# Kernel tuning notes

Measured on AMD Instinct MI355X. Metric: run time of the kernel, lower is better.

Reference implementation:

```python
import jax, jax.numpy as jnp
import numpy as np

EPS = 1e-5
NEG = -1e9

def rmsnorm(x, g, eps=EPS):
    x32 = x.astype(jnp.float32)
    n = x32 * jax.lax.rsqrt(jnp.mean(x32 * x32, axis=-1, keepdims=True) + eps)
    return g * n.astype(x.dtype)

def setup_inputs() -> dict:
    key = jax.random.key(0)
    ks = jax.random.split(key, 10)
    B, S, D, H = 2, 2048, 768, 12
    F = 4 * D
    s = 0.02
    return {
        "x": jax.random.normal(ks[0], (B, S, D), jnp.float32),
        "mask": jax.random.randint(ks[1], (B, S, S), 0, 2, jnp.int32),
        "wq": jax.random.normal(ks[2], (D, D), jnp.float32) * s,
        "wk": jax.random.normal(ks[3], (D, D), jnp.float32) * s,
        "wv": jax.random.normal(ks[4], (D, D), jnp.float32) * s,
        "wo": jax.random.normal(ks[5], (D, D), jnp.float32) * s,
        "w1": jax.random.normal(ks[6], (F, D), jnp.float32) * s,
        "w2": jax.random.normal(ks[7], (D, F), jnp.float32) * s,
        "w3": jax.random.normal(ks[8], (F, D), jnp.float32) * s,
        "g_attn": jnp.ones((D,), jnp.float32),
        "g_ffn": jnp.ones((D,), jnp.float32),
    }

def reference(x, mask, wq, wk, wv, wo, w1, w2, w3, g_attn, g_ffn):
    B, S, D = x.shape
    H = 12
    Dk = D // H
    # --- attention sub-block (pre-norm) ---
    xn = rmsnorm(x, g_attn)
    # torch Linear: y = x @ W^T; split heads -> [B,H,S,Dk]
    q = (xn @ wq.T).reshape(B, S, H, Dk).transpose(0, 2, 1, 3)
    k = (xn @ wk.T).reshape(B, S, H, Dk).transpose(0, 2, 1, 3)
    v = (xn @ wv.T).reshape(B, S, H, Dk).transpose(0, 2, 1, 3)
    scores = jnp.einsum("bhqd,bhkd->bhqk", q, k) / jnp.sqrt(jnp.float32(Dk))
    scores = jnp.where(mask[:, None, :, :] == 0, jnp.float32(NEG), scores)
    probs = jax.nn.softmax(scores, axis=-1)  # dropout p=0.0 -> identity
    attn = jnp.einsum("bhqk,bhkd->bhqd", probs, v)
    attn = attn.transpose(0, 2, 1, 3).reshape(B, S, D)
    h = x + attn @ wo.T
    # --- SwiGLU FFN sub-block (pre-norm) ---
    hn = rmsnorm(h, g_ffn)
    ffn = (jax.nn.silu(hn @ w1.T) * (hn @ w3.T)) @ w2.T
    return h + ffn
```

## Files before the change

### kernel.cpp

```cpp
#include <hip/hip_runtime.h>
#include <hip/hip_bf16.h>

#define S_LEN 2048
#define D_MODEL 768
#define NH 12
#define DK 64
#define F_DIM 3072
#define BATCH 2
#define M_ROWS (BATCH * S_LEN)

typedef __bf16 bf16x8 __attribute__((ext_vector_type(8)));
typedef float floatx4 __attribute__((ext_vector_type(4)));
typedef unsigned short u16;
typedef unsigned long long u64;

__device__ inline float bf2f(u16 u) {
    union { unsigned int i; float f; } x; x.i = ((unsigned int)u) << 16; return x.f;
}
__device__ inline u16 f2bf(float f) {
    union { float f; unsigned int i; } x; x.f = f;
    unsigned int r = x.i + 0x7fffu + ((x.i >> 16) & 1u);
    return (u16)(r >> 16);
}
__device__ __forceinline__ bf16x8 as_bf16x8(uint4 v) {
    union { uint4 u; bf16x8 b; } c; c.u = v; return c.b;
}

__device__ __forceinline__ void ldsload16(const u16* g, u16* l) {
    __builtin_amdgcn_global_load_lds(
        (const __attribute__((address_space(1))) unsigned int*)g,
        (__attribute__((address_space(3))) unsigned int*)l, 16, 0, 0);
}

__global__ __launch_bounds__(256)
void cvt_all(const float4* __restrict__ wq, const float4* __restrict__ wk,
             const float4* __restrict__ wv, const float4* __restrict__ wo,
             const float4* __restrict__ w1, const float4* __restrict__ w2,
             const float4* __restrict__ w3,
             ushort4* wqb, ushort4* wkb, ushort4* wvb, ushort4* wob,
             ushort4* w13f, ushort4* w2b) {
    const int WS4 = (D_MODEL * D_MODEL) / 4;
    const int WB4 = (F_DIM * D_MODEL) / 4;
    const int RW4 = D_MODEL / 4;
    int i = blockIdx.x * 256 + threadIdx.x;
    const float4* src; ushort4* dst; int off, doff;
    if (i < 4 * WS4) {
        int s = i / WS4; off = i - s * WS4; doff = off;
        src = (s == 0) ? wq : (s == 1) ? wk : (s == 2) ? wv : wo;
        dst = (s == 0) ? wqb : (s == 1) ? wkb : (s == 2) ? wvb : wob;
    } else {
        int j = i - 4 * WS4; int s = j / WB4; off = j - s * WB4;
        if (s == 1) { src = w2; dst = w2b; doff = off; }
        else {
            src = (s == 0) ? w1 : w3;
            dst = w13f;
            int which = (s == 0) ? 0 : 1;
            int row = off / RW4, c4 = off - row * RW4;
            int k = c4 * 4;
            int n_tile = row >> 4, nl = row & 15;
            int k_tile = k >> 5, quad = (k >> 3) & 3, jj = k & 7;
            int lane = quad * 16 + nl;
            int f = (n_tile * 24 + k_tile) * 2 + which;
            doff = (f * 512 + lane * 8 + jj) >> 2;
        }
    }
    float4 v = src[off];
    ushort4 o;
    o.x = f2bf(v.x); o.y = f2bf(v.y); o.z = f2bf(v.z); o.w = f2bf(v.w);
    dst[doff] = o;
}

__global__ __launch_bounds__(256)
void mask_bits(const int* __restrict__ m, u64* __restrict__ bits) {
    size_t base = (size_t)blockIdx.x * 2048 + threadIdx.x;
    #pragma unroll
    for (int it = 0; it < 8; ++it) {
        size_t gid = base + (size_t)it * 256;
        u64 b = __ballot(m[gid] != 0);
        if ((threadIdx.x & 63) == 0) bits[gid >> 6] = b;
    }
}

__global__ __launch_bounds__(256)
void rmsnorm_k(const float* __restrict__ x, const float* __restrict__ g, u16* __restrict__ out) {
    int row = blockIdx.x;
    const float* xr = x + (size_t)row * D_MODEL;
    u16* orow = out + (size_t)row * D_MODEL;
    int t = threadIdx.x;
    float v0 = xr[t];
    float v1 = xr[t + 256];
    float v2 = xr[t + 512];
    float ss = v0 * v0 + v1 * v1 + v2 * v2;
    #pragma unroll
    for (int off = 1; off < 64; off <<= 1) ss += __shfl_xor(ss, off);
    __shared__ float red[4];
    if ((t & 63) == 0) red[t >> 6] = ss;
    __syncthreads();
    float tot = red[0] + red[1] + red[2] + red[3];
    float scale = rsqrtf(tot * (1.0f / (float)D_MODEL) + 1e-5f);
    orow[t]       = f2bf(g[t]       * v0 * scale);
    orow[t + 256] = f2bf(g[t + 256] * v1 * scale);
    orow[t + 512] = f2bf(g[t + 512] * v2 * scale);
}

__global__ __launch_bounds__(256, 3)
void gemm_f1(const u16* __restrict__ A, const u16* __restrict__ W13f,
             u16* __restrict__ Cout) {
    const int K = D_MODEL, N = F_DIM;
    __shared__ u16 As[2][64][64];

    int t = threadIdx.x;
    int w = t >> 6, lane = t & 63;
    int lrow = lane & 15, quad = lane >> 4;

    int lid = blockIdx.y * 24 + blockIdx.x;
    int xcd = lid & 7, s = lid >> 3;
    int nb = xcd * 3 + (s % 3);
    int mb = s / 3;
    int mBase = mb * 64;
    int ntile0 = nb * 8 + w * 2;

    int srow8 = lane >> 3;
    int sc64 = ((lane & 7) ^ srow8) * 8;
    const u16* Ag = A + (size_t)(mBase + w * 16 + srow8) * K + sc64;
    const uint4* Bf = (const uint4*)W13f;

    auto stageA = [&](int k0, int b) {
        ldsload16(Ag + k0,                 &As[b][w * 16][0]);
        ldsload16(Ag + (size_t)8 * K + k0, &As[b][w * 16 + 8][0]);
    };

    floatx4 zero = {0.f, 0.f, 0.f, 0.f};
    floatx4 acc[4][2], acc2[4][2];
    #pragma unroll
    for (int r = 0; r < 4; ++r)
        #pragma unroll
        for (int c = 0; c < 2; ++c) { acc[r][c] = zero; acc2[r][c] = zero; }

    stageA(0, 0);
    int cur = 0;
    for (int kt2 = 0; kt2 < 12; ++kt2) {
        uint4 b1v[2][2], b3v[2][2];
        #pragma unroll
        for (int hh = 0; hh < 2; ++hh) {
            int kt = kt2 * 2 + hh;
            #pragma unroll
            for (int c = 0; c < 2; ++c) {
                int f = ((ntile0 + c) * 24 + kt) * 2;
                b1v[hh][c] = Bf[(size_t)f * 64 + lane];
                b3v[hh][c] = Bf[(size_t)(f + 1) * 64 + lane];
            }
        }
        __syncthreads();
        if (kt2 + 1 < 12) stageA((kt2 + 1) * 64, cur ^ 1);

        #pragma unroll
        for (int hh = 0; hh < 2; ++hh) {
            int rc = ((hh * 4 + quad) ^ (lrow & 7)) * 8;
            bf16x8 af[4];
            #pragma unroll
            for (int r = 0; r < 4; ++r) af[r] = *(const bf16x8*)&As[cur][r * 16 + lrow][rc];
            #pragma unroll
            for (int c = 0; c < 2; ++c) {
                bf16x8 b1f = as_bf16x8(b1v[hh][c]);
                bf16x8 b3f = as_bf16x8(b3v[hh][c]);
                #pragma unroll
                for (int r = 0; r < 4; ++r) {
                    acc[r][c]  = __builtin_amdgcn_mfma_f32_16x16x32_bf16(af[r], b1f, acc[r][c], 0, 0, 0);
                    acc2[r][c] = __builtin_amdgcn_mfma_f32_16x16x32_bf16(af[r], b3f, acc2[r][c], 0, 0, 0);
                }
            }
        }
        cur ^= 1;
    }

    #pragma unroll
    for (int r = 0; r < 4; ++r) {
        #pragma unroll
        for (int c = 0; c < 2; ++c) {
            #pragma unroll
            for (int j = 0; j < 4; ++j) {
                int grow = mBase + r * 16 + quad * 4 + j;
                int gcol = nb * 128 + w * 32 + c * 16 + lrow;
                float a = acc[r][c][j];
                Cout[(size_t)grow * N + gcol] = f2bf((a / (1.0f + __expf(-a))) * acc2[r][c][j]);
            }
        }
    }
}

__global__ __launch_bounds__(256, 3)
void gemm64(const u16* __restrict__ A, const u16* __restrict__ B1,
            const float* __restrict__ R, float* __restrict__ Cout, int N, int K) {
    __shared__ u16 As[2][64][64];
    __shared__ u16 Bs[2][64][64];

    int t = threadIdx.x;
    int w = t >> 6, lane = t & 63;

    int L = blockIdx.y * gridDim.x + blockIdx.x;
    int xcd = L & 7;
    int i = L >> 3;
    int nT = gridDim.x;
    int mPer = gridDim.y >> 3;
    int nIdx = i % nT;
    int mIdx = xcd * mPer + i / nT;
    int mBase = mIdx * 64, nBase = nIdx * 64;

    int lrow = lane & 15, quad = lane >> 4;
    int wm = (w >> 1) * 32, wn = (w & 1) * 32;

    int srow8 = lane >> 3;
    int sc64 = ((lane & 7) ^ srow8) * 8;
    const u16* Ag = A  + (size_t)(mBase + w * 16 + srow8) * K + sc64;
    const u16* Bg = B1 + (size_t)(nBase + w * 16 + srow8) * K + sc64;

    auto stage = [&](int k0, int b) {
        ldsload16(Ag + k0,                 &As[b][w * 16][0]);
        ldsload16(Ag + (size_t)8 * K + k0, &As[b][w * 16 + 8][0]);
        ldsload16(Bg + k0,                 &Bs[b][w * 16][0]);
        ldsload16(Bg + (size_t)8 * K + k0, &Bs[b][w * 16 + 8][0]);
    };

    floatx4 zero = {0.f, 0.f, 0.f, 0.f};
    floatx4 acc[2][2];
    #pragma unroll
    for (int r = 0; r < 2; ++r)
        #pragma unroll
        for (int c = 0; c < 2; ++c) acc[r][c] = zero;

    stage(0, 0);
    int cur = 0;
    for (int k0 = 0; k0 < K; k0 += 64) {
        __syncthreads();
        if (k0 + 64 < K) stage(k0 + 64, cur ^ 1);

        #pragma unroll
        for (int half = 0; half < 2; ++half) {
            int rc = ((half * 4 + quad) ^ (lrow & 7)) * 8;
            bf16x8 af[2], bf[2];
            #pragma unroll
            for (int r = 0; r < 2; ++r) af[r] = *(const bf16x8*)&As[cur][wm + r * 16 + lrow][rc];
            #pragma unroll
            for (int c = 0; c < 2; ++c) bf[c] = *(const bf16x8*)&Bs[cur][wn + c * 16 + lrow][rc];
            #pragma unroll
            for (int r = 0; r < 2; ++r)
                #pragma unroll
                for (int c = 0; c < 2; ++c)
                    acc[r][c] = __builtin_amdgcn_mfma_f32_16x16x32_bf16(af[r], bf[c], acc[r][c], 0, 0, 0);
        }
        cur ^= 1;
    }

    #pragma unroll
    for (int r = 0; r < 2; ++r) {
        #pragma unroll
        for (int c = 0; c < 2; ++c) {
            #pragma unroll
            for (int j = 0; j < 4; ++j) {
                int grow = mBase + wm + r * 16 + quad * 4 + j;
                int gcol = nBase + wn + c * 16 + lrow;
                size_t idx = (size_t)grow * N + gcol;
                Cout[idx] = acc[r][c][j] + R[idx];
            }
        }
    }
}

__global__ __launch_bounds__(256, 4)
void gemm_qkv(const u16* __restrict__ A, const u16* __restrict__ wq,
              const u16* __restrict__ wk, const u16* __restrict__ wv,
              u16* __restrict__ qb, u16* __restrict__ kb, u16* __restrict__ vt) {
    const int K = D_MODEL;
    __shared__ u16 As[2][64][32];
    __shared__ u16 Bs[2][128][32];

    int t = threadIdx.x;
    int w = t >> 6, lane = t & 63;

    int L = blockIdx.y * 18 + blockIdx.x;
    int g = (L & 7) * 144 + (L >> 3);
    int xI = g >> 6;
    int yI = g & 63;
    int which = xI / 6;
    int mBase = yI * 64, nBase = (xI % 6) * 128;
    const u16* B1 = (which == 0) ? wq : (which == 1) ? wk : wv;
    int lrow = lane & 15, quad = lane >> 4;
    int wm = (w >> 1) * 32, wn = (w & 1) * 64;

    int srow = lane >> 2;
    int scolS = ((lane & 3) ^ ((lane >> 3) & 3)) * 8;
    int rq = (quad ^ ((lrow >> 1) & 3)) * 8;
    const u16* Ag = A  + (size_t)(mBase + w * 16 + srow) * K + scolS;
    const u16* Bg = B1 + (size_t)(nBase + w * 32 + srow) * K + scolS;

    auto stage = [&](int k0, int b) {
        ldsload16(Ag + k0, &As[b][w * 16][0]);
        ldsload16(Bg + k0, &Bs[b][w * 32][0]);
        ldsload16(Bg + (size_t)16 * K + k0, &Bs[b][w * 32 + 16][0]);
    };

    floatx4 zero = {0.f, 0.f, 0.f, 0.f};
    floatx4 acc[2][4];
    #pragma unroll
    for (int r = 0; r < 2; ++r)
        #pragma unroll
        for (int c = 0; c < 4; ++c) acc[r][c] = zero;

    stage(0, 0);
    int cur = 0;
    for (int k0 = 0; k0 < K; k0 += 32) {
        __syncthreads();
        if (k0 + 32 < K) stage(k0 + 32, cur ^ 1);
        bf16x8 af[2];
        #pragma unroll
        for (int r = 0; r < 2; ++r) af[r] = *(const bf16x8*)&As[cur][wm + r * 16 + lrow][rq];
        #pragma unroll
        for (int c = 0; c < 4; ++c) {
            bf16x8 bfr = *(const bf16x8*)&Bs[cur][wn + c * 16 + lrow][rq];
            #pragma unroll
            for (int r = 0; r < 2; ++r)
                acc[r][c] = __builtin_amdgcn_mfma_f32_16x16x32_bf16(af[r], bfr, acc[r][c], 0, 0, 0);
        }
        cur ^= 1;
    }

    u16* dst = (which == 0) ? qb : kb;
    const float qscale = 0.18033688011112042f;
    #pragma unroll
    for (int r = 0; r < 2; ++r) {
        #pragma unroll
        for (int c = 0; c < 4; ++c) {
            #pragma unroll
            for (int j = 0; j < 4; ++j) {
                int grow = mBase + wm + r * 16 + quad * 4 + j;
                int gcol = nBase + wn + c * 16 + lrow;
                float val = acc[r][c][j];
                if (which == 2) {
                    int bb = grow >> 11, s = grow & 2047;
                    int hh = gcol >> 6, d = gcol & 63;
                    vt[((((size_t)bb * NH + hh) * DK + d) << 11) + s] = f2bf(val);
                } else {
                    if (which == 0) val *= qscale;
                    dst[(size_t)grow * D_MODEL + gcol] = f2bf(val);
                }
            }
        }
    }
}

__global__ __launch_bounds__(256)
void attn_mfma(const u16* __restrict__ q, const u16* __restrict__ k,
               const u16* __restrict__ vt, const u64* __restrict__ mbits,
               u16* __restrict__ out) {
    __shared__ u16 Ks0[2][64][32], Ks1[2][64][32];
    __shared__ u16 Vs0[2][64][32], Vs1[2][64][32];
    __shared__ u16 PT[4][16][64];

    int t = threadIdx.x;
    int lane = t & 63;
    int w = t >> 6;
    int lrow = lane & 15;
    int quad = lane >> 4;

    int L = blockIdx.y * gridDim.x + blockIdx.x;
    int g = (L & 7) * 96 + (L >> 3);
    int st0 = (g & 31) * 64;
    int bh = g >> 5;
    int h = bh % NH;
    int b = bh / NH;

    const u16* kbase = k + (size_t)b * S_LEN * D_MODEL + h * DK;
    const u16* vbase = vt + (size_t)bh * DK * S_LEN;
    const u64* bw = mbits + ((size_t)b * S_LEN + st0 + w * 16 + lrow) * (S_LEN / 64);

    int srow = lane >> 2;
    int scolS = ((lane & 3) ^ ((lane >> 3) & 3)) * 8;
    int rq = (quad ^ ((lrow >> 1) & 3)) * 8;
    int ptw = lrow & 7;
    int rp0 = (quad ^ ptw) * 8;
    int rp1 = ((4 + quad) ^ ptw) * 8;
    int pqo = (quad & 1) * 4;
    int pch = quad >> 1;

    const u16* kg = kbase + (size_t)(w * 16 + srow) * D_MODEL + scolS;
    const u16* vg = vbase + (size_t)(w * 16 + srow) * S_LEN + scolS;

    auto stageKV = [&](int kt, int bsel) {
        ldsload16(kg + (size_t)kt * D_MODEL,      &Ks0[bsel][w * 16][0]);
        ldsload16(kg + (size_t)kt * D_MODEL + 32, &Ks1[bsel][w * 16][0]);
        ldsload16(vg + kt,      &Vs0[bsel][w * 16][0]);
        ldsload16(vg + kt + 32, &Vs1[bsel][w * 16][0]);
    };

    stageKV(0, 0);

    bf16x8 bq0, bq1;
    {
        const u16* qrow = q + ((size_t)b * S_LEN + st0 + w * 16 + lrow) * D_MODEL + h * DK + quad * 8;
        bq0 = *(const bf16x8*)qrow;
        bq1 = *(const bf16x8*)(qrow + 32);
    }

    bf16x8 ones;
    {
        union { u16 u; __bf16 b; } o; o.u = 0x3F80;
        #pragma unroll
        for (int j = 0; j < 8; ++j) ones[j] = o.b;
    }

    floatx4 zero = {0.f, 0.f, 0.f, 0.f};
    floatx4 Ot[4] = {zero, zero, zero, zero};
    floatx4 Osum = zero;

    u64 mw = bw[0];
    __syncthreads();

    int cur = 0;
    for (int kt = 0; kt < S_LEN; kt += 64) {
        if (kt + 64 < S_LEN) stageKV(kt + 64, cur ^ 1);
        u64 mw_next = (kt + 64 < S_LEN) ? bw[(kt >> 6) + 1] : 0ull;
        unsigned mlo = (unsigned)mw, mhi = (unsigned)(mw >> 32);

        floatx4 st[4];
        #pragma unroll
        for (int nt = 0; nt < 4; ++nt) {
            bf16x8 ak0 = *(const bf16x8*)&Ks0[cur][nt * 16 + lrow][rq];
            bf16x8 ak1 = *(const bf16x8*)&Ks1[cur][nt * 16 + lrow][rq];
            st[nt] = __builtin_amdgcn_mfma_f32_16x16x32_bf16(ak0, bq0, zero, 0, 0, 0);
            st[nt] = __builtin_amdgcn_mfma_f32_16x16x32_bf16(ak1, bq1, st[nt], 0, 0, 0);
        }

        #pragma unroll
        for (int nt = 0; nt < 4; ++nt) {
            unsigned half = (nt & 2) ? mhi : mlo;
            unsigned tmp = half >> ((nt & 1) * 16 + quad * 4);
            unsigned eu[4];
            #pragma unroll
            for (int j = 0; j < 4; ++j) {
                float e = __builtin_amdgcn_exp2f(st[nt][j]);
                unsigned msk = (unsigned)((int)(tmp << (31 - j)) >> 31);
                eu[j] = __float_as_uint(e) & msk;
            }
            uint2 p;
            p.x = (eu[0] >> 16) | (eu[1] & 0xffff0000u);
            p.y = (eu[2] >> 16) | (eu[3] & 0xffff0000u);
            int pc = ((nt * 2 + pch) ^ ptw) * 8 + pqo;
            *(uint2*)&PT[w][lrow][pc] = p;
        }

        bf16x8 ap0 = *(const bf16x8*)&PT[w][lrow][rp0];
        bf16x8 ap1 = *(const bf16x8*)&PT[w][lrow][rp1];
        Osum = __builtin_amdgcn_mfma_f32_16x16x32_bf16(ap0, ones, Osum, 0, 0, 0);
        Osum = __builtin_amdgcn_mfma_f32_16x16x32_bf16(ap1, ones, Osum, 0, 0, 0);
        #pragma unroll
        for (int dt = 0; dt < 4; ++dt) {
            bf16x8 bv0 = *(const bf16x8*)&Vs0[cur][dt * 16 + lrow][rq];
            bf16x8 bv1 = *(const bf16x8*)&Vs1[cur][dt * 16 + lrow][rq];
            Ot[dt] = __builtin_amdgcn_mfma_f32_16x16x32_bf16(ap0, bv0, Ot[dt], 0, 0, 0);
            Ot[dt] = __builtin_amdgcn_mfma_f32_16x16x32_bf16(ap1, bv1, Ot[dt], 0, 0, 0);
        }

        __syncthreads();
        cur ^= 1;
        mw = mw_next;
    }

    float invj[4];
    #pragma unroll
    for (int j = 0; j < 4; ++j) invj[j] = 1.0f / Osum[j];

    u16* obase = out + ((size_t)b * S_LEN + st0 + w * 16) * D_MODEL + h * DK;
    #pragma unroll
    for (int dt = 0; dt < 4; ++dt)
        #pragma unroll
        for (int j = 0; j < 4; ++j)
            obase[(size_t)(quad * 4 + j) * D_MODEL + dt * 16 + lrow] = f2bf(Ot[dt][j] * invj[j]);
}

extern "C" void kernel_launch(void* const* d_in, const int* in_sizes, int n_in,
                              void* d_out, int out_size, void* d_ws, size_t ws_size,
                              hipStream_t stream) {
    const float* x      = (const float*)d_in[0];
    const int*   mask   = (const int*)d_in[1];
    const float* wq     = (const float*)d_in[2];
    const float* wk     = (const float*)d_in[3];
    const float* wv     = (const float*)d_in[4];
    const float* wo     = (const float*)d_in[5];
    const float* w1     = (const float*)d_in[6];
    const float* w2     = (const float*)d_in[7];
    const float* w3     = (const float*)d_in[8];
    const float* g_attn = (const float*)d_in[9];
    const float* g_ffn  = (const float*)d_in[10];
    float* out = (float*)d_out;

    const size_t WSMALL = (size_t)D_MODEL * D_MODEL;
    const size_t WBIG   = (size_t)F_DIM * D_MODEL;
    const size_t MD     = (size_t)M_ROWS * D_MODEL;

    char* ws = (char*)d_ws;
    u16* wqb  = (u16*)ws;            ws += WSMALL * 2;
    u16* wkb  = (u16*)ws;            ws += WSMALL * 2;
    u16* wvb  = (u16*)ws;            ws += WSMALL * 2;
    u16* wob  = (u16*)ws;            ws += WSMALL * 2;
    u16* w13f = (u16*)ws;            ws += WBIG * 2 * 2;
    u16* w2b  = (u16*)ws;            ws += WBIG * 2;
    u16* xn  = (u16*)ws;             ws += MD * 2;
    u16* qb  = (u16*)ws;             ws += MD * 2;
    u16* kb  = (u16*)ws;             ws += MD * 2;
    u16* vb  = (u16*)ws;             ws += MD * 2;
    u16* ao  = (u16*)ws;             ws += MD * 2;
    float* hb = (float*)ws;          ws += MD * 4;
    u64* mb  = (u64*)ws;             ws += (size_t)BATCH * S_LEN * (S_LEN / 64) * 8;
    u16* hn = xn;
    u16* ub = qb;
    (void)ws_size; (void)n_in; (void)in_sizes; (void)out_size;

    dim3 blk(256);

    cvt_all<<<9216, blk, 0, stream>>>((const float4*)wq, (const float4*)wk, (const float4*)wv,
                                      (const float4*)wo, (const float4*)w1, (const float4*)w2,
                                      (const float4*)w3,
                                      (ushort4*)wqb, (ushort4*)wkb, (ushort4*)wvb, (ushort4*)wob,
                                      (ushort4*)w13f, (ushort4*)w2b);
    mask_bits<<<(BATCH * S_LEN * S_LEN) / 2048, blk, 0, stream>>>(mask, mb);

    rmsnorm_k<<<M_ROWS, blk, 0, stream>>>(x, g_attn, xn);
    gemm_qkv<<<dim3(18, M_ROWS / 64), blk, 0, stream>>>(xn, wqb, wkb, wvb, qb, kb, vb);
    attn_mfma<<<dim3(S_LEN / 64, BATCH * NH), blk, 0, stream>>>(qb, kb, vb, mb, ao);
    gemm64<<<dim3(D_MODEL / 64, M_ROWS / 64), blk, 0, stream>>>(ao, wob, x, hb, D_MODEL, D_MODEL);
    rmsnorm_k<<<M_ROWS, blk, 0, stream>>>((const float*)hb, g_ffn, hn);
    gemm_f1<<<dim3(24, M_ROWS / 64), blk, 0, stream>>>(hn, w13f, ub);
    gemm64<<<dim3(D_MODEL / 64, M_ROWS / 64), blk, 0, stream>>>(ub, w2b, hb, out, D_MODEL, F_DIM);
}
```

Baseline: 327.6 us.

## Merge prep kernels and switch QKV GEMM to fragment-packed weights

The weight conversion, mask bit-packing and first RMSNorm now run as one combined launch, so two kernel launches and their gaps disappear. Wq/Wk/Wv are converted into one MFMA-fragment-ordered buffer. The QKV GEMM then loads B fragments straight from global memory into registers, with no LDS staging, and stages only A through LDS with a 64-wide K tile and XOR swizzle. This trades LDS traffic and barriers for direct global loads of B, and changes the warp tiling to 64x32 per warp.

```diff
diff --git a/kernel.cpp b/kernel.cpp
--- a/kernel.cpp
+++ b/kernel.cpp
@@ -32,22 +32,30 @@
         (__attribute__((address_space(3))) unsigned int*)l, 16, 0, 0);
 }
 
-__global__ __launch_bounds__(256)
-void cvt_all(const float4* __restrict__ wq, const float4* __restrict__ wk,
-             const float4* __restrict__ wv, const float4* __restrict__ wo,
-             const float4* __restrict__ w1, const float4* __restrict__ w2,
-             const float4* __restrict__ w3,
-             ushort4* wqb, ushort4* wkb, ushort4* wvb, ushort4* wob,
-             ushort4* w13f, ushort4* w2b) {
+__device__ __forceinline__ void cvt_body(
+        int i,
+        const float4* wq, const float4* wk, const float4* wv, const float4* wo,
+        const float4* w1, const float4* w2, const float4* w3,
+        ushort4* wqkvf, ushort4* wob, ushort4* w13f, ushort4* w2b) {
     const int WS4 = (D_MODEL * D_MODEL) / 4;
     const int WB4 = (F_DIM * D_MODEL) / 4;
     const int RW4 = D_MODEL / 4;
-    int i = blockIdx.x * 256 + threadIdx.x;
     const float4* src; ushort4* dst; int off, doff;
     if (i < 4 * WS4) {
-        int s = i / WS4; off = i - s * WS4; doff = off;
+        int s = i / WS4; off = i - s * WS4;
         src = (s == 0) ? wq : (s == 1) ? wk : (s == 2) ? wv : wo;
-        dst = (s == 0) ? wqb : (s == 1) ? wkb : (s == 2) ? wvb : wob;
+        if (s == 3) { dst = wob; doff = off; }
+        else {
+            dst = wqkvf;
+            int row = off / RW4, c4 = off - row * RW4;
+            int k = c4 * 4;
+            int rg = s * D_MODEL + row;
+            int n_tile = rg >> 4, nl = rg & 15;
+            int k_tile = k >> 5, qd = (k >> 3) & 3, jj = k & 7;
+            int ln = qd * 16 + nl;
+            int f = n_tile * 24 + k_tile;
+            doff = (f * 512 + ln * 8 + jj) >> 2;
+        }
     } else {
         int j = i - 4 * WS4; int s = j / WB4; off = j - s * WB4;
         if (s == 1) { src = w2; dst = w2b; doff = off; }
@@ -58,10 +66,10 @@
             int row = off / RW4, c4 = off - row * RW4;
             int k = c4 * 4;
             int n_tile = row >> 4, nl = row & 15;
-            int k_tile = k >> 5, quad = (k >> 3) & 3, jj = k & 7;
-            int lane = quad * 16 + nl;
+            int k_tile = k >> 5, qd = (k >> 3) & 3, jj = k & 7;
+            int ln = qd * 16 + nl;
             int f = (n_tile * 24 + k_tile) * 2 + which;
-            doff = (f * 512 + lane * 8 + jj) >> 2;
+            doff = (f * 512 + ln * 8 + jj) >> 2;
         }
     }
     float4 v = src[off];
@@ -70,9 +78,8 @@
     dst[doff] = o;
 }
 
-__global__ __launch_bounds__(256)
-void mask_bits(const int* __restrict__ m, u64* __restrict__ bits) {
-    size_t base = (size_t)blockIdx.x * 2048 + threadIdx.x;
+__device__ __forceinline__ void mask_body(int bx, const int* m, u64* bits) {
+    size_t base = (size_t)bx * 2048 + threadIdx.x;
     #pragma unroll
     for (int it = 0; it < 8; ++it) {
         size_t gid = base + (size_t)it * 256;
@@ -81,9 +88,8 @@
     }
 }
 
-__global__ __launch_bounds__(256)
-void rmsnorm_k(const float* __restrict__ x, const float* __restrict__ g, u16* __restrict__ out) {
-    int row = blockIdx.x;
+__device__ __forceinline__ void rms_body(int row, const float* x, const float* g,
+                                         u16* out, float* red) {
     const float* xr = x + (size_t)row * D_MODEL;
     u16* orow = out + (size_t)row * D_MODEL;
     int t = threadIdx.x;
@@ -93,7 +99,6 @@
     float ss = v0 * v0 + v1 * v1 + v2 * v2;
     #pragma unroll
     for (int off = 1; off < 64; off <<= 1) ss += __shfl_xor(ss, off);
-    __shared__ float red[4];
     if ((t & 63) == 0) red[t >> 6] = ss;
     __syncthreads();
     float tot = red[0] + red[1] + red[2] + red[3];
@@ -101,6 +106,30 @@
     orow[t]       = f2bf(g[t]       * v0 * scale);
     orow[t + 256] = f2bf(g[t + 256] * v1 * scale);
     orow[t + 512] = f2bf(g[t + 512] * v2 * scale);
+}
+
+__global__ __launch_bounds__(256)
+void prep(const float4* wq, const float4* wk, const float4* wv, const float4* wo,
+          const float4* w1, const float4* w2, const float4* w3,
+          ushort4* wqkvf, ushort4* wob, ushort4* w13f, ushort4* w2b,
+          const int* m, u64* bits,
+          const float* x, const float* g, u16* xn) {
+    __shared__ float red[4];
+    int bx = blockIdx.x;
+    if (bx < 9216) {
+        cvt_body(bx * 256 + threadIdx.x, wq, wk, wv, wo, w1, w2, w3,
+                 wqkvf, wob, w13f, w2b);
+    } else if (bx < 13312) {
+        mask_body(bx - 9216, m, bits);
+    } else {
+        rms_body(bx - 13312, x, g, xn, red);
+    }
+}
+
+__global__ __launch_bounds__(256)
+void rmsnorm_k(const float* __restrict__ x, const float* __restrict__ g, u16* __restrict__ out) {
+    __shared__ float red[4];
+    rms_body(blockIdx.x, x, g, out, red);
 }
 
 __global__ __launch_bounds__(256, 3)
@@ -268,81 +297,91 @@
 }
 
 __global__ __launch_bounds__(256, 4)
-void gemm_qkv(const u16* __restrict__ A, const u16* __restrict__ wq,
-              const u16* __restrict__ wk, const u16* __restrict__ wv,
+void gemm_qkv(const u16* __restrict__ A, const u16* __restrict__ Wf,
               u16* __restrict__ qb, u16* __restrict__ kb, u16* __restrict__ vt) {
     const int K = D_MODEL;
-    __shared__ u16 As[2][64][32];
-    __shared__ u16 Bs[2][128][32];
+    __shared__ u16 As[2][64][64];
 
     int t = threadIdx.x;
     int w = t >> 6, lane = t & 63;
+    int lrow = lane & 15, quad = lane >> 4;
 
     int L = blockIdx.y * 18 + blockIdx.x;
     int g = (L & 7) * 144 + (L >> 3);
-    int xI = g >> 6;
-    int yI = g & 63;
-    int which = xI / 6;
-    int mBase = yI * 64, nBase = (xI % 6) * 128;
-    const u16* B1 = (which == 0) ? wq : (which == 1) ? wk : wv;
-    int lrow = lane & 15, quad = lane >> 4;
-    int wm = (w >> 1) * 32, wn = (w & 1) * 64;
-
-    int srow = lane >> 2;
-    int scolS = ((lane & 3) ^ ((lane >> 3) & 3)) * 8;
-    int rq = (quad ^ ((lrow >> 1) & 3)) * 8;
-    const u16* Ag = A  + (size_t)(mBase + w * 16 + srow) * K + scolS;
-    const u16* Bg = B1 + (size_t)(nBase + w * 32 + srow) * K + scolS;
-
-    auto stage = [&](int k0, int b) {
-        ldsload16(Ag + k0, &As[b][w * 16][0]);
-        ldsload16(Bg + k0, &Bs[b][w * 32][0]);
-        ldsload16(Bg + (size_t)16 * K + k0, &Bs[b][w * 32 + 16][0]);
+    int nb = g >> 6;
+    int mBase = (g & 63) * 64;
+    int ntile0 = nb * 8 + w * 2;
+
+    int srow8 = lane >> 3;
+    int sc64 = ((lane & 7) ^ srow8) * 8;
+    const u16* Ag = A + (size_t)(mBase + w * 16 + srow8) * K + sc64;
+    const uint4* Bf = (const uint4*)Wf;
+
+    auto stageA = [&](int k0, int b) {
+        ldsload16(Ag + k0,                 &As[b][w * 16][0]);
+        ldsload16(Ag + (size_t)8 * K + k0, &As[b][w * 16 + 8][0]);
     };
 
     floatx4 zero = {0.f, 0.f, 0.f, 0.f};
-    floatx4 acc[2][4];
-    #pragma unroll
-    for (int r = 0; r < 2; ++r)
-        #pragma unroll
-        for (int c = 0; c < 4; ++c) acc[r][c] = zero;
-
-    stage(0, 0);
+    floatx4 acc[4][2];
+    #pragma unroll
+    for (int r = 0; r < 4; ++r)
+        #pragma unroll
+        for (int c = 0; c < 2; ++c) acc[r][c] = zero;
+
+    stageA(0, 0);
     int cur = 0;
-    for (int k0 = 0; k0 < K; k0 += 32) {
+    for (int kt2 = 0; kt2 < 12; ++kt2) {
+        uint4 bv[2][2];
+        #pragma unroll
+        for (int hh = 0; hh < 2; ++hh) {
+            int kt = kt2 * 2 + hh;
+            #pragma unroll
+            for (int c = 0; c < 2; ++c) {
+                int f = (ntile0 + c) * 24 + kt;
+                bv[hh][c] = Bf[(size_t)f * 64 + lane];
+            }
+        }
         __syncthreads();
-        if (k0 + 32 < K) stage(k0 + 32, cur ^ 1);
-        bf16x8 af[2];
-        #pragma unroll
-        for (int r = 0; r < 2; ++r) af[r] = *(const bf16x8*)&As[cur][wm + r * 16 + lrow][rq];
-        #pragma unroll
-        for (int c = 0; c < 4; ++c) {
-            bf16x8 bfr = *(const bf16x8*)&Bs[cur][wn + c * 16 + lrow][rq];
-            #pragma unroll
-            for (int r = 0; r < 2; ++r)
-                acc[r][c] = __builtin_amdgcn_mfma_f32_16x16x32_bf16(af[r], bfr, acc[r][c], 0, 0, 0);
+        if (kt2 + 1 < 12) stageA((kt2 + 1) * 64, cur ^ 1);
+
+        #pragma unroll
+        for (int hh = 0; hh < 2; ++hh) {
+            int rc = ((hh * 4 + quad) ^ (lrow & 7)) * 8;
+            bf16x8 af[4];
+            #pragma unroll
+            for (int r = 0; r < 4; ++r) af[r] = *(const bf16x8*)&As[cur][r * 16 + lrow][rc];
+            #pragma unroll
+            for (int c = 0; c < 2; ++c) {
+                bf16x8 bfr = as_bf16x8(bv[hh][c]);
+                #pragma unroll
+                for (int r = 0; r < 4; ++r)
+                    acc[r][c] = __builtin_amdgcn_mfma_f32_16x16x32_bf16(af[r], bfr, acc[r][c], 0, 0, 0);
+            }
         }
         cur ^= 1;
     }
 
+    const float qscale = 0.18033688011112042f;
+    int which = nb / 6;
     u16* dst = (which == 0) ? qb : kb;
-    const float qscale = 0.18033688011112042f;
-    #pragma unroll
-    for (int r = 0; r < 2; ++r) {
-        #pragma unroll
-        for (int c = 0; c < 4; ++c) {
+    #pragma unroll
+    for (int r = 0; r < 4; ++r) {
+        #pragma unroll
+        for (int c = 0; c < 2; ++c) {
             #pragma unroll
             for (int j = 0; j < 4; ++j) {
-                int grow = mBase + wm + r * 16 + quad * 4 + j;
-                int gcol = nBase + wn + c * 16 + lrow;
+                int grow = mBase + r * 16 + quad * 4 + j;
+                int gcol = nb * 128 + w * 32 + c * 16 + lrow;
+                int cm = gcol - which * D_MODEL;
                 float val = acc[r][c][j];
                 if (which == 2) {
                     int bb = grow >> 11, s = grow & 2047;
-                    int hh = gcol >> 6, d = gcol & 63;
+                    int hh = cm >> 6, d = cm & 63;
                     vt[((((size_t)bb * NH + hh) * DK + d) << 11) + s] = f2bf(val);
                 } else {
                     if (which == 0) val *= qscale;
-                    dst[(size_t)grow * D_MODEL + gcol] = f2bf(val);
+                    dst[(size_t)grow * D_MODEL + cm] = f2bf(val);
                 }
             }
         }
@@ -499,9 +538,7 @@
     const size_t MD     = (size_t)M_ROWS * D_MODEL;
 
     char* ws = (char*)d_ws;
-    u16* wqb  = (u16*)ws;            ws += WSMALL * 2;
-    u16* wkb  = (u16*)ws;            ws += WSMALL * 2;
-    u16* wvb  = (u16*)ws;            ws += WSMALL * 2;
+    u16* wqkvf = (u16*)ws;           ws += WSMALL * 3 * 2;
     u16* wob  = (u16*)ws;            ws += WSMALL * 2;
     u16* w13f = (u16*)ws;            ws += WBIG * 2 * 2;
     u16* w2b  = (u16*)ws;            ws += WBIG * 2;
@@ -518,15 +555,13 @@
 
     dim3 blk(256);
 
-    cvt_all<<<9216, blk, 0, stream>>>((const float4*)wq, (const float4*)wk, (const float4*)wv,
-                                      (const float4*)wo, (const float4*)w1, (const float4*)w2,
-                                      (const float4*)w3,
-                                      (ushort4*)wqb, (ushort4*)wkb, (ushort4*)wvb, (ushort4*)wob,
-                                      (ushort4*)w13f, (ushort4*)w2b);
-    mask_bits<<<(BATCH * S_LEN * S_LEN) / 2048, blk, 0, stream>>>(mask, mb);
-
-    rmsnorm_k<<<M_ROWS, blk, 0, stream>>>(x, g_attn, xn);
-    gemm_qkv<<<dim3(18, M_ROWS / 64), blk, 0, stream>>>(xn, wqb, wkb, wvb, qb, kb, vb);
+    prep<<<17408, blk, 0, stream>>>((const float4*)wq, (const float4*)wk, (const float4*)wv,
+                                    (const float4*)wo, (const float4*)w1, (const float4*)w2,
+                                    (const float4*)w3,
+                                    (ushort4*)wqkvf, (ushort4*)wob, (ushort4*)w13f, (ushort4*)w2b,
+                                    mask, mb, x, g_attn, xn);
+
+    gemm_qkv<<<dim3(18, M_ROWS / 64), blk, 0, stream>>>(xn, wqkvf, qb, kb, vb);
     attn_mfma<<<dim3(S_LEN / 64, BATCH * NH), blk, 0, stream>>>(qb, kb, vb, mb, ao);
     gemm64<<<dim3(D_MODEL / 64, M_ROWS / 64), blk, 0, stream>>>(ao, wob, x, hb, D_MODEL, D_MODEL);
     rmsnorm_k<<<M_ROWS, blk, 0, stream>>>((const float*)hb, g_ffn, hn);
```

After: 325.9 us. No clear change (-0.5%).
